# Kernel optimization log

Measured on AMD Instinct MI355X. Metric: run time of the kernel, lower is better.

Reference implementation:

```python
import jax, jax.numpy as jnp
import numpy as np

N_NODES = 50000


def _sage_conv(x, src, dst, Wl, bl, Wr):
    # mean aggregation of source-node features into target nodes
    agg = jax.ops.segment_sum(x[src], dst, num_segments=N_NODES)      # [N, C]
    deg = jax.ops.segment_sum(jnp.ones_like(src, dtype=x.dtype), dst,
                              num_segments=N_NODES)                   # [N]
    mean = agg / jnp.maximum(deg, 1.0)[:, None]
    # PyG SAGEConv: lin_l(aggr) (with bias) + lin_r(x) (no bias)
    return mean @ Wl.T + bl + x @ Wr.T


def setup_inputs() -> dict:
    key = jax.random.key(0)
    ks = jax.random.split(key, 8)
    C = 128
    E = 600000
    scale = 1.0 / np.sqrt(C)
    x = jax.random.normal(ks[0], (N_NODES, C), dtype=jnp.float32)
    edge_index = jax.random.randint(ks[1], (2, E), 0, N_NODES, dtype=jnp.int64)
    Wl1 = jax.random.normal(ks[2], (C, C), dtype=jnp.float32) * scale
    bl1 = jnp.zeros((C,), dtype=jnp.float32)
    Wr1 = jax.random.normal(ks[3], (C, C), dtype=jnp.float32) * scale
    Wl2 = jax.random.normal(ks[4], (C, C), dtype=jnp.float32) * scale
    bl2 = jnp.zeros((C,), dtype=jnp.float32)
    Wr2 = jax.random.normal(ks[5], (C, C), dtype=jnp.float32) * scale
    return {"x": x, "edge_index": edge_index, "Wl1": Wl1, "bl1": bl1,
            "Wr1": Wr1, "Wl2": Wl2, "bl2": bl2, "Wr2": Wr2}


def reference(x, edge_index, Wl1, bl1, Wr1, Wl2, bl2, Wr2):
    src, dst = edge_index[0], edge_index[1]
    h = _sage_conv(x, src, dst, Wl1, bl1, Wr1)
    h = jax.nn.relu(h)
    out = _sage_conv(h, src, dst, Wl2, bl2, Wr2)
    return out
```

## Files before the change

kernel.cpp:

```cpp
#include <hip/hip_runtime.h>

#define N_NODES 50000
#define C 128
#define FB_ROWS 16
#define FUSED_BLOCKS (N_NODES / FB_ROWS)
#define XPREP_BLOCKS 3125
#define WPREP_BLOCKS 256
#define CAP 48
#define CSTRIDE 32
#define FPITCH 132
#define DEGQ 8

typedef short bf16x8 __attribute__((ext_vector_type(8)));
typedef float f32x4 __attribute__((ext_vector_type(4)));
typedef float f32x2 __attribute__((ext_vector_type(2)));

#if defined(__has_builtin)
#if __has_builtin(__builtin_amdgcn_cvt_pk_f32_fp8)
#define HAVE_FP8_DEC 1
#endif
#if __has_builtin(__builtin_amdgcn_cvt_pk_fp8_f32)
#define HAVE_FP8_ENC 1
#endif
#endif

__device__ __forceinline__ unsigned short f2bf(float f) {
    unsigned int u = __float_as_uint(f);
    unsigned int r = u + 0x7fffu + ((u >> 16) & 1u);
    return (unsigned short)(r >> 16);
}

__device__ __forceinline__ float bf2f(unsigned short b) {
    return __uint_as_float(((unsigned int)b) << 16);
}

__device__ __forceinline__ unsigned char f32_to_fp8(float v) {
#ifdef HAVE_FP8_ENC
    return (unsigned char)(__builtin_amdgcn_cvt_pk_fp8_f32(v, v, 0u, false) & 0xFFu);
#else
    unsigned int u = __float_as_uint(v);
    unsigned int s = (u >> 24) & 0x80u;
    unsigned int av = u & 0x7fffffffu;
    if (av >= 0x43e00000u) return (unsigned char)(s | 0x7Eu);
    if (av < 0x3c800000u) {
        float af = __uint_as_float(av);
        int m = (int)(af * 512.0f + 0.5f);
        return (unsigned char)(s | (unsigned)m);
    }
    unsigned int r = av + 0x7ffffu + ((av >> 20) & 1u);
    unsigned int e = (r >> 23) - 120u;
    unsigned int m = (r >> 20) & 7u;
    if (e > 15u) { e = 15u; m = 6u; }
    return (unsigned char)(s | (e << 3) | m);
#endif
}

__device__ __forceinline__ float fp8_to_f32(unsigned int b) {
    unsigned int e = (b >> 3) & 0xFu;
    unsigned int m = b & 7u;
    float f = (e == 0) ? (float)m * 0.001953125f
                       : __uint_as_float(((e + 120u) << 23) | (m << 20));
    return (b & 0x80u) ? -f : f;
}

__device__ __forceinline__ void acc8(float* a, uint4 u) {
    const unsigned int uu[4] = {u.x, u.y, u.z, u.w};
#pragma unroll
    for (int i = 0; i < 4; ++i) {
        a[2 * i] += bf2f((unsigned short)uu[i]);
        a[2 * i + 1] += bf2f((unsigned short)(uu[i] >> 16));
    }
}

__device__ __forceinline__ void acc8q(float* a, uint2 u) {
#ifdef HAVE_FP8_DEC
    f32x2 p;
    p = __builtin_amdgcn_cvt_pk_f32_fp8(u.x, false); a[0] += p[0]; a[1] += p[1];
    p = __builtin_amdgcn_cvt_pk_f32_fp8(u.x, true);  a[2] += p[0]; a[3] += p[1];
    p = __builtin_amdgcn_cvt_pk_f32_fp8(u.y, false); a[4] += p[0]; a[5] += p[1];
    p = __builtin_amdgcn_cvt_pk_f32_fp8(u.y, true);  a[6] += p[0]; a[7] += p[1];
#else
#pragma unroll
    for (int i = 0; i < 4; ++i) a[i] += fp8_to_f32((u.x >> (8 * i)) & 0xFFu);
#pragma unroll
    for (int i = 0; i < 4; ++i) a[4 + i] += fp8_to_f32((u.y >> (8 * i)) & 0xFFu);
#endif
}

__global__ __launch_bounds__(256) void buildfill_kernel(
    const int* __restrict__ src, const int* __restrict__ dst, int E, int edgeBlocks,
    int* __restrict__ cursor, int* __restrict__ csr,
    const float* __restrict__ x, unsigned short* __restrict__ Xb,
    unsigned char* __restrict__ Xq,
    const float* __restrict__ Wl1, const float* __restrict__ Wr1,
    const float* __restrict__ Wl2, const float* __restrict__ Wr2,
    unsigned short* __restrict__ Wc1, unsigned short* __restrict__ Wc2) {
    int b = blockIdx.x;
    if (b < edgeBlocks) {
        int e = b * 256 + threadIdx.x;
        if (e < E) {
            int d = dst[e];
            int s = src[e];
            if ((unsigned)d < (unsigned)N_NODES && (unsigned)s < (unsigned)N_NODES) {
                int slot = atomicAdd(cursor + d * CSTRIDE, 1);
                if (slot < CAP) csr[d * CAP + slot] = s;
            }
        }
    } else if (b < edgeBlocks + XPREP_BLOCKS) {
        int t = (b - edgeBlocks) * 256 + threadIdx.x;
        if (t >= N_NODES * C / 8) return;
        const float4 a = *(const float4*)(x + (size_t)t * 8);
        const float4 c = *(const float4*)(x + (size_t)t * 8 + 4);
        unsigned short o[8] = {f2bf(a.x), f2bf(a.y), f2bf(a.z), f2bf(a.w),
                               f2bf(c.x), f2bf(c.y), f2bf(c.z), f2bf(c.w)};
        *(uint4*)(Xb + (size_t)t * 8) = *(const uint4*)o;
        unsigned char q[8] = {f32_to_fp8(a.x), f32_to_fp8(a.y), f32_to_fp8(a.z), f32_to_fp8(a.w),
                              f32_to_fp8(c.x), f32_to_fp8(c.y), f32_to_fp8(c.z), f32_to_fp8(c.w)};
        *(uint2*)(Xq + (size_t)t * 8) = *(const uint2*)q;
    } else {
        int idx = (b - edgeBlocks - XPREP_BLOCKS) * 256 + threadIdx.x;
        int layer = idx >> 15;
        int r = idx & 32767;
        int j = r >> 8, k = r & 255;
        const float* Wl = layer ? Wl2 : Wl1;
        const float* Wr = layer ? Wr2 : Wr1;
        unsigned short* Wc = layer ? Wc2 : Wc1;
        float f = (k < 128) ? Wl[j * 128 + k] : Wr[j * 128 + (k - 128)];
        Wc[r] = f2bf(f);
    }
}

__global__ __launch_bounds__(256, 4) void sage_fused16(
    const unsigned short* __restrict__ feat,
    const unsigned char* __restrict__ featq,
    const int* __restrict__ cursor, const int* __restrict__ csr,
    const unsigned short* __restrict__ Wc,
    const float* __restrict__ bias,
    void* __restrict__ outv, unsigned char* __restrict__ outq,
    int relu, int obf16) {
    __shared__ unsigned short fm[FB_ROWS * FPITCH];

    const int lane = threadIdx.x & 63;
    const int w = threadIdx.x >> 6;
    const int g = lane >> 4;
    const int c = lane & 15;
    const int base = blockIdx.x * FB_ROWS;
    const unsigned short* fp = feat + c * 8;
    const unsigned char* fq = featq + c * 8;

    const int n0 = base + w * 4;
    int degr[4], idx[4];
#pragma unroll
    for (int i = 0; i < 4; ++i) degr[i] = cursor[(size_t)(n0 + i) * CSTRIDE];
#pragma unroll
    for (int i = 0; i < 4; ++i) idx[i] = (lane < CAP) ? csr[(n0 + i) * CAP + lane] : 0;

#pragma unroll 1
    for (int i = 0; i < 4; ++i) {
        const int deg = min(degr[i], CAP);
        const int myidx = idx[i];
        float a[8];
#pragma unroll
        for (int k = 0; k < 8; ++k) a[k] = 0.f;

        if (deg >= DEGQ) {
            const int nb = (deg + 3) >> 2;
            uint2 u[6];
#pragma unroll
            for (int b = 0; b < 6; ++b) {
                if (b < nb) {
                    int r = 4 * b + g;
                    int s = __shfl(myidx, r < deg ? r : 0);
                    u[b] = *(const uint2*)(fq + (size_t)s * C);
                }
            }
#pragma unroll
            for (int b = 0; b < 6; ++b)
                if (b < nb && 4 * b + g < deg) acc8q(a, u[b]);
            if (nb > 6) {
                for (int b = 6; b < nb; ++b) {
                    int r = 4 * b + g;
                    int s = __shfl(myidx, r < deg ? r : 0);
                    uint2 uu = *(const uint2*)(fq + (size_t)s * C);
                    if (r < deg) acc8q(a, uu);
                }
            }
        } else {
            const int nb = (deg + 3) >> 2;
            uint4 u[2];
#pragma unroll
            for (int b = 0; b < 2; ++b) {
                if (b < nb) {
                    int r = 4 * b + g;
                    int s = __shfl(myidx, r < deg ? r : 0);
                    u[b] = *(const uint4*)(fp + (size_t)s * C);
                }
            }
#pragma unroll
            for (int b = 0; b < 2; ++b)
                if (b < nb && 4 * b + g < deg) acc8(a, u[b]);
        }
#pragma unroll
        for (int k = 0; k < 8; ++k) {
            a[k] += __shfl_xor(a[k], 16);
            a[k] += __shfl_xor(a[k], 32);
        }
        const float inv = 1.0f / fmaxf((float)deg, 1.0f);
        if (g == 0) {
            unsigned int o[4];
#pragma unroll
            for (int k = 0; k < 4; ++k)
                o[k] = (unsigned)f2bf(a[2 * k] * inv) |
                       ((unsigned)f2bf(a[2 * k + 1] * inv) << 16);
            *(uint4*)(&fm[(w * 4 + i) * FPITCH + c * 8]) = *(const uint4*)o;
        }
    }
    __syncthreads();

    const unsigned short* as = feat + (size_t)(base + c) * C + g * 8;
    f32x4 acc2[2];
    acc2[0] = (f32x4){0.f, 0.f, 0.f, 0.f};
    acc2[1] = (f32x4){0.f, 0.f, 0.f, 0.f};
#pragma unroll
    for (int kt = 0; kt < 8; ++kt) {
        bf16x8 af;
        if (kt < 4)
            af = *(const bf16x8*)(&fm[c * FPITCH + kt * 32 + g * 8]);
        else
            af = *(const bf16x8*)(as + (kt & 3) * 32);
#pragma unroll
        for (int j = 0; j < 2; ++j) {
            bf16x8 bfrag = *(const bf16x8*)(Wc + ((w * 2 + j) * 16 + c) * 256 + kt * 32 + g * 8);
            acc2[j] = __builtin_amdgcn_mfma_f32_16x16x32_bf16(af, bfrag, acc2[j], 0, 0, 0);
        }
    }
#pragma unroll
    for (int j = 0; j < 2; ++j) {
        const int col = (w * 2 + j) * 16 + c;
        const float bcol = bias[col];
#pragma unroll
        for (int r = 0; r < 4; ++r) {
            const int row = base + g * 4 + r;
            float v = acc2[j][r] + bcol;
            if (relu) v = fmaxf(v, 0.0f);
            if (obf16)
                ((unsigned short*)outv)[(size_t)row * C + col] = f2bf(v);
            else
                ((float*)outv)[(size_t)row * C + col] = v;
            if (outq)
                outq[(size_t)row * C + col] = f32_to_fp8(v);
        }
    }
}

extern "C" void kernel_launch(void* const* d_in, const int* in_sizes, int n_in,
                              void* d_out, int out_size, void* d_ws, size_t ws_size,
                              hipStream_t stream) {
    const float* x = (const float*)d_in[0];
    const int* edge = (const int*)d_in[1];
    const float* Wl1 = (const float*)d_in[2];
    const float* bl1 = (const float*)d_in[3];
    const float* Wr1 = (const float*)d_in[4];
    const float* Wl2 = (const float*)d_in[5];
    const float* bl2 = (const float*)d_in[6];
    const float* Wr2 = (const float*)d_in[7];
    float* out = (float*)d_out;

    const int E = in_sizes[1] / 2;
    const int* src = edge;
    const int* dst = edge + E;

    char* ws = (char*)d_ws;
    size_t off = 0;
    int* cursor = (int*)(ws + off);           off += (size_t)N_NODES * CSTRIDE * 4;
    off = (off + 511) & ~511ull;
    int* csr = (int*)(ws + off);              off += (size_t)N_NODES * CAP * 4;
    off = (off + 511) & ~511ull;
    unsigned short* Xb = (unsigned short*)(ws + off); off += (size_t)N_NODES * C * 2;
    unsigned short* h  = (unsigned short*)(ws + off); off += (size_t)N_NODES * C * 2;
    unsigned char* Xq = (unsigned char*)(ws + off);   off += (size_t)N_NODES * C;
    unsigned char* hq = (unsigned char*)(ws + off);   off += (size_t)N_NODES * C;
    unsigned short* Wc1 = (unsigned short*)(ws + off); off += 128 * 256 * 2;
    unsigned short* Wc2 = (unsigned short*)(ws + off); off += 128 * 256 * 2;
    (void)ws_size;

    const int edgeBlocks = (E + 255) / 256;

    hipMemsetAsync(cursor, 0, (size_t)N_NODES * CSTRIDE * 4, stream);
    buildfill_kernel<<<edgeBlocks + XPREP_BLOCKS + WPREP_BLOCKS, 256, 0, stream>>>(
        src, dst, E, edgeBlocks, cursor, csr, x, Xb, Xq, Wl1, Wr1, Wl2, Wr2, Wc1, Wc2);

    sage_fused16<<<FUSED_BLOCKS, 256, 0, stream>>>(
        Xb, Xq, cursor, csr, Wc1, bl1, h, hq, 1, 1);

    sage_fused16<<<FUSED_BLOCKS, 256, 0, stream>>>(
        h, hq, cursor, csr, Wc2, bl2, out, (unsigned char*)nullptr, 0, 0);
}
```

Before: 208.6 us.

## Widen fp8 gathers to 16 bytes per lane and overlap self-term MFMA with aggregation

The fp8 neighbor-gather path now has each lane load 16 bytes (8 lanes per row, 8 rows in flight per wave) instead of 8 bytes, halving the number of gather iterations and adding one extra butterfly reduction step. The self-feature operand for the root-weight half of the GEMM is loaded at kernel start, and its MFMAs are issued before the barrier so they overlap the gather and reduction phase. Register pressure rises because of the 16-wide accumulators and the prefetched self fragments, which may reduce occupancy under the 4-blocks launch bound.

```diff
diff --git a/kernel.cpp b/kernel.cpp
--- a/kernel.cpp
+++ b/kernel.cpp
@@ -72,18 +72,24 @@
     }
 }
 
-__device__ __forceinline__ void acc8q(float* a, uint2 u) {
+__device__ __forceinline__ void acc16q(float* a, uint4 u) {
 #ifdef HAVE_FP8_DEC
     f32x2 p;
-    p = __builtin_amdgcn_cvt_pk_f32_fp8(u.x, false); a[0] += p[0]; a[1] += p[1];
-    p = __builtin_amdgcn_cvt_pk_f32_fp8(u.x, true);  a[2] += p[0]; a[3] += p[1];
-    p = __builtin_amdgcn_cvt_pk_f32_fp8(u.y, false); a[4] += p[0]; a[5] += p[1];
-    p = __builtin_amdgcn_cvt_pk_f32_fp8(u.y, true);  a[6] += p[0]; a[7] += p[1];
+    p = __builtin_amdgcn_cvt_pk_f32_fp8(u.x, false); a[0] += p[0];  a[1] += p[1];
+    p = __builtin_amdgcn_cvt_pk_f32_fp8(u.x, true);  a[2] += p[0];  a[3] += p[1];
+    p = __builtin_amdgcn_cvt_pk_f32_fp8(u.y, false); a[4] += p[0];  a[5] += p[1];
+    p = __builtin_amdgcn_cvt_pk_f32_fp8(u.y, true);  a[6] += p[0];  a[7] += p[1];
+    p = __builtin_amdgcn_cvt_pk_f32_fp8(u.z, false); a[8] += p[0];  a[9] += p[1];
+    p = __builtin_amdgcn_cvt_pk_f32_fp8(u.z, true);  a[10] += p[0]; a[11] += p[1];
+    p = __builtin_amdgcn_cvt_pk_f32_fp8(u.w, false); a[12] += p[0]; a[13] += p[1];
+    p = __builtin_amdgcn_cvt_pk_f32_fp8(u.w, true);  a[14] += p[0]; a[15] += p[1];
 #else
-#pragma unroll
-    for (int i = 0; i < 4; ++i) a[i] += fp8_to_f32((u.x >> (8 * i)) & 0xFFu);
-#pragma unroll
-    for (int i = 0; i < 4; ++i) a[4 + i] += fp8_to_f32((u.y >> (8 * i)) & 0xFFu);
+    const unsigned int uu[4] = {u.x, u.y, u.z, u.w};
+#pragma unroll
+    for (int q = 0; q < 4; ++q)
+#pragma unroll
+        for (int i = 0; i < 4; ++i)
+            a[q * 4 + i] += fp8_to_f32((uu[q] >> (8 * i)) & 0xFFu);
 #endif
 }
 
@@ -144,9 +150,17 @@
     const int w = threadIdx.x >> 6;
     const int g = lane >> 4;
     const int c = lane & 15;
+    const int g8 = lane >> 3;
+    const int c8 = lane & 7;
     const int base = blockIdx.x * FB_ROWS;
     const unsigned short* fp = feat + c * 8;
-    const unsigned char* fq = featq + c * 8;
+    const unsigned char* fq = featq + c8 * 16;
+
+    const unsigned short* as = feat + (size_t)(base + c) * C + g * 8;
+    const bf16x8 s0 = *(const bf16x8*)(as + 0);
+    const bf16x8 s1 = *(const bf16x8*)(as + 32);
+    const bf16x8 s2 = *(const bf16x8*)(as + 64);
+    const bf16x8 s3 = *(const bf16x8*)(as + 96);
 
     const int n0 = base + w * 4;
     int degr[4], idx[4];
@@ -159,33 +173,53 @@
     for (int i = 0; i < 4; ++i) {
         const int deg = min(degr[i], CAP);
         const int myidx = idx[i];
-        float a[8];
-#pragma unroll
-        for (int k = 0; k < 8; ++k) a[k] = 0.f;
+        const float inv = 1.0f / fmaxf((float)deg, 1.0f);
 
         if (deg >= DEGQ) {
-            const int nb = (deg + 3) >> 2;
-            uint2 u[6];
-#pragma unroll
-            for (int b = 0; b < 6; ++b) {
+            float a[16];
+#pragma unroll
+            for (int k = 0; k < 16; ++k) a[k] = 0.f;
+            const int nb = (deg + 7) >> 3;
+            uint4 u[3];
+#pragma unroll
+            for (int b = 0; b < 3; ++b) {
                 if (b < nb) {
-                    int r = 4 * b + g;
+                    int r = 8 * b + g8;
                     int s = __shfl(myidx, r < deg ? r : 0);
-                    u[b] = *(const uint2*)(fq + (size_t)s * C);
+                    u[b] = *(const uint4*)(fq + (size_t)s * C);
                 }
             }
 #pragma unroll
-            for (int b = 0; b < 6; ++b)
-                if (b < nb && 4 * b + g < deg) acc8q(a, u[b]);
-            if (nb > 6) {
-                for (int b = 6; b < nb; ++b) {
-                    int r = 4 * b + g;
+            for (int b = 0; b < 3; ++b)
+                if (b < nb && 8 * b + g8 < deg) acc16q(a, u[b]);
+            if (nb > 3) {
+                for (int b = 3; b < nb; ++b) {
+                    int r = 8 * b + g8;
                     int s = __shfl(myidx, r < deg ? r : 0);
-                    uint2 uu = *(const uint2*)(fq + (size_t)s * C);
-                    if (r < deg) acc8q(a, uu);
+                    uint4 uu = *(const uint4*)(fq + (size_t)s * C);
+                    if (r < deg) acc16q(a, uu);
                 }
             }
+#pragma unroll
+            for (int k = 0; k < 16; ++k) {
+                a[k] += __shfl_xor(a[k], 8);
+                a[k] += __shfl_xor(a[k], 16);
+                a[k] += __shfl_xor(a[k], 32);
+            }
+            if (g8 == 0) {
+                unsigned int o[8];
+#pragma unroll
+                for (int k = 0; k < 8; ++k)
+                    o[k] = (unsigned)f2bf(a[2 * k] * inv) |
+                           ((unsigned)f2bf(a[2 * k + 1] * inv) << 16);
+                unsigned short* dstp = &fm[(w * 4 + i) * FPITCH + c8 * 16];
+                *(uint4*)dstp = *(const uint4*)o;
+                *(uint4*)(dstp + 8) = *(const uint4*)(o + 4);
+            }
         } else {
+            float a[8];
+#pragma unroll
+            for (int k = 0; k < 8; ++k) a[k] = 0.f;
             const int nb = (deg + 3) >> 2;
             uint4 u[2];
 #pragma unroll
@@ -199,38 +233,41 @@
 #pragma unroll
             for (int b = 0; b < 2; ++b)
                 if (b < nb && 4 * b + g < deg) acc8(a, u[b]);
+#pragma unroll
+            for (int k = 0; k < 8; ++k) {
+                a[k] += __shfl_xor(a[k], 16);
+                a[k] += __shfl_xor(a[k], 32);
+            }
+            if (g == 0) {
+                unsigned int o[4];
+#pragma unroll
+                for (int k = 0; k < 4; ++k)
+                    o[k] = (unsigned)f2bf(a[2 * k] * inv) |
+                           ((unsigned)f2bf(a[2 * k + 1] * inv) << 16);
+                *(uint4*)(&fm[(w * 4 + i) * FPITCH + c * 8]) = *(const uint4*)o;
+            }
         }
-#pragma unroll
-        for (int k = 0; k < 8; ++k) {
-            a[k] += __shfl_xor(a[k], 16);
-            a[k] += __shfl_xor(a[k], 32);
-        }
-        const float inv = 1.0f / fmaxf((float)deg, 1.0f);
-        if (g == 0) {
-            unsigned int o[4];
-#pragma unroll
-            for (int k = 0; k < 4; ++k)
-                o[k] = (unsigned)f2bf(a[2 * k] * inv) |
-                       ((unsigned)f2bf(a[2 * k + 1] * inv) << 16);
-            *(uint4*)(&fm[(w * 4 + i) * FPITCH + c * 8]) = *(const uint4*)o;
-        }
-    }
-    __syncthreads();
-
-    const unsigned short* as = feat + (size_t)(base + c) * C + g * 8;
+    }
+
     f32x4 acc2[2];
     acc2[0] = (f32x4){0.f, 0.f, 0.f, 0.f};
     acc2[1] = (f32x4){0.f, 0.f, 0.f, 0.f};
 #pragma unroll
-    for (int kt = 0; kt < 8; ++kt) {
-        bf16x8 af;
-        if (kt < 4)
-            af = *(const bf16x8*)(&fm[c * FPITCH + kt * 32 + g * 8]);
-        else
-            af = *(const bf16x8*)(as + (kt & 3) * 32);
+    for (int j = 0; j < 2; ++j) {
+        const unsigned short* wb = Wc + ((w * 2 + j) * 16 + c) * 256 + g * 8;
+        acc2[j] = __builtin_amdgcn_mfma_f32_16x16x32_bf16(s0, *(const bf16x8*)(wb + 4 * 32), acc2[j], 0, 0, 0);
+        acc2[j] = __builtin_amdgcn_mfma_f32_16x16x32_bf16(s1, *(const bf16x8*)(wb + 5 * 32), acc2[j], 0, 0, 0);
+        acc2[j] = __builtin_amdgcn_mfma_f32_16x16x32_bf16(s2, *(const bf16x8*)(wb + 6 * 32), acc2[j], 0, 0, 0);
+        acc2[j] = __builtin_amdgcn_mfma_f32_16x16x32_bf16(s3, *(const bf16x8*)(wb + 7 * 32), acc2[j], 0, 0, 0);
+    }
+    __syncthreads();
+
+#pragma unroll
+    for (int kt = 0; kt < 4; ++kt) {
+        const bf16x8 af = *(const bf16x8*)(&fm[c * FPITCH + kt * 32 + g * 8]);
 #pragma unroll
         for (int j = 0; j < 2; ++j) {
-            bf16x8 bfrag = *(const bf16x8*)(Wc + ((w * 2 + j) * 16 + c) * 256 + kt * 32 + g * 8);
+            const bf16x8 bfrag = *(const bf16x8*)(Wc + ((w * 2 + j) * 16 + c) * 256 + kt * 32 + g * 8);
             acc2[j] = __builtin_amdgcn_mfma_f32_16x16x32_bf16(af, bfrag, acc2[j], 0, 0, 0);
         }
     }
```

Result: slower. 220.2 us (+5.6%).

## Shard per-node edge cursors into four sub-buckets to reduce atomic contention

Applied to the files above, without the earlier changes.

Each destination node's adjacency bucket is split into four sub-buckets chosen by edge index, each with its own padded atomic cursor and 24-slot capacity. The goal is to spread atomic conflicts on hot nodes. The fused aggregation kernel now reads four cursors per node and computes prefix offsets so each lane can gather its neighbor index from the right sub-bucket. In exchange, the cursor array and its memset grow fourfold, and every node needs more cursor loads.

```diff
diff --git a/kernel.cpp b/kernel.cpp
--- a/kernel.cpp
+++ b/kernel.cpp
@@ -6,7 +6,8 @@
 #define FUSED_BLOCKS (N_NODES / FB_ROWS)
 #define XPREP_BLOCKS 3125
 #define WPREP_BLOCKS 256
-#define CAP 48
+#define NSUB 4
+#define CAPS 24
 #define CSTRIDE 32
 #define FPITCH 132
 #define DEGQ 8
@@ -102,8 +103,9 @@
             int d = dst[e];
             int s = src[e];
             if ((unsigned)d < (unsigned)N_NODES && (unsigned)s < (unsigned)N_NODES) {
-                int slot = atomicAdd(cursor + d * CSTRIDE, 1);
-                if (slot < CAP) csr[d * CAP + slot] = s;
+                int sub = e & (NSUB - 1);
+                int slot = atomicAdd(cursor + ((size_t)d * NSUB + sub) * CSTRIDE, 1);
+                if (slot < CAPS) csr[((size_t)d * NSUB + sub) * CAPS + slot] = s;
             }
         }
     } else if (b < edgeBlocks + XPREP_BLOCKS) {
@@ -149,15 +151,32 @@
     const unsigned char* fq = featq + c * 8;
 
     const int n0 = base + w * 4;
+    int cs0[4], cs1[4], cs2[4], cs3[4];
+#pragma unroll
+    for (int i = 0; i < 4; ++i) {
+        cs0[i] = cursor[((size_t)(n0 + i) * NSUB + 0) * CSTRIDE];
+        cs1[i] = cursor[((size_t)(n0 + i) * NSUB + 1) * CSTRIDE];
+        cs2[i] = cursor[((size_t)(n0 + i) * NSUB + 2) * CSTRIDE];
+        cs3[i] = cursor[((size_t)(n0 + i) * NSUB + 3) * CSTRIDE];
+    }
     int degr[4], idx[4];
 #pragma unroll
-    for (int i = 0; i < 4; ++i) degr[i] = cursor[(size_t)(n0 + i) * CSTRIDE];
-#pragma unroll
-    for (int i = 0; i < 4; ++i) idx[i] = (lane < CAP) ? csr[(n0 + i) * CAP + lane] : 0;
+    for (int i = 0; i < 4; ++i) {
+        const int c0 = min(cs0[i], CAPS), c1 = min(cs1[i], CAPS);
+        const int c2 = min(cs2[i], CAPS), c3 = min(cs3[i], CAPS);
+        const int p1 = c0, p2 = c0 + c1, p3 = c0 + c1 + c2;
+        degr[i] = p3 + c3;
+        const int sub = (lane >= p1 ? 1 : 0) + (lane >= p2 ? 1 : 0) + (lane >= p3 ? 1 : 0);
+        int off = lane - (sub == 0 ? 0 : (sub == 1 ? p1 : (sub == 2 ? p2 : p3)));
+        off = min(off, CAPS - 1);
+        idx[i] = (lane < degr[i])
+                     ? csr[((size_t)(n0 + i) * NSUB + sub) * CAPS + off]
+                     : 0;
+    }
 
 #pragma unroll 1
     for (int i = 0; i < 4; ++i) {
-        const int deg = min(degr[i], CAP);
+        const int deg = degr[i];
         const int myidx = idx[i];
         float a[8];
 #pragma unroll
@@ -272,9 +291,9 @@
 
     char* ws = (char*)d_ws;
     size_t off = 0;
-    int* cursor = (int*)(ws + off);           off += (size_t)N_NODES * CSTRIDE * 4;
+    int* cursor = (int*)(ws + off);           off += (size_t)N_NODES * NSUB * CSTRIDE * 4;
     off = (off + 511) & ~511ull;
-    int* csr = (int*)(ws + off);              off += (size_t)N_NODES * CAP * 4;
+    int* csr = (int*)(ws + off);              off += (size_t)N_NODES * NSUB * CAPS * 4 + 512;
     off = (off + 511) & ~511ull;
     unsigned short* Xb = (unsigned short*)(ws + off); off += (size_t)N_NODES * C * 2;
     unsigned short* h  = (unsigned short*)(ws + off); off += (size_t)N_NODES * C * 2;
@@ -286,7 +305,7 @@
 
     const int edgeBlocks = (E + 255) / 256;
 
-    hipMemsetAsync(cursor, 0, (size_t)N_NODES * CSTRIDE * 4, stream);
+    hipMemsetAsync(cursor, 0, (size_t)N_NODES * NSUB * CSTRIDE * 4, stream);
     buildfill_kernel<<<edgeBlocks + XPREP_BLOCKS + WPREP_BLOCKS, 256, 0, stream>>>(
         src, dst, E, edgeBlocks, cursor, csr, x, Xb, Xq, Wl1, Wr1, Wl2, Wr2, Wc1, Wc2);
 
```

Measured after the change: 219.4 us. +5.2%, slower.
